# Kernel tuning notes

Hardware: AMD Instinct MI355X
Metric: run time of the kernel (lower is better)

Reference implementation:

```python
import jax, jax.numpy as jnp
import numpy as np
from jax import lax

B, T, C = 1, 2048, 2048
HS = 64
H = C // HS          # 32 heads
FFN = 7168
NS = 4               # packed sequences in the batch-1 stream
EPS_LN = 1e-5
EPS_GN = 1e-5 * 8 ** 2   # GroupNorm eps = 1e-5 * head_size_divisor**2


def setup_inputs() -> dict:
    key = jax.random.key(0)
    ks = iter(jax.random.split(key, 48))
    def rn(shape, s=1.0):
        return jax.random.normal(next(ks), shape, jnp.float32) * s
    sc = C ** -0.5
    return dict(
        x=rn((B, T, C)),
        start_pos=jnp.array([0, 512, 1024, 1536], dtype=jnp.int32),
        att_state=rn((NS, C)),
        wkv_state=rn((NS, H, HS, HS), 0.1),
        ffn_state=rn((NS, C)),
        ln1_g=jnp.ones((C,), jnp.float32), ln1_b=jnp.zeros((C,), jnp.float32),
        ln2_g=jnp.ones((C,), jnp.float32), ln2_b=jnp.zeros((C,), jnp.float32),
        tm_maa_x=rn((C,), 0.1), tm_maa_w=rn((C,), 0.1), tm_maa_k=rn((C,), 0.1),
        tm_maa_v=rn((C,), 0.1), tm_maa_r=rn((C,), 0.1), tm_maa_g=rn((C,), 0.1),
        tm_w1=rn((C, 160), 0.02), tm_w2=rn((5, 32, C), 0.02),
        td=rn((C,), 0.3) - 0.5, td_w1=rn((C, 64), 0.02), td_w2=rn((64, C), 0.02),
        u=rn((H, HS), 0.1),
        Wr=rn((C, C), sc), Wk=rn((C, C), sc), Wv=rn((C, C), sc),
        Wg=rn((C, C), sc), Wo=rn((C, C), sc),
        lnx_g=jnp.ones((C,), jnp.float32), lnx_b=jnp.zeros((C,), jnp.float32),
        cm_maa_k=rn((C,), 0.1), cm_maa_r=rn((C,), 0.1),
        Wck=rn((C, FFN), sc), Wcv=rn((FFN, C), FFN ** -0.5), Wcr=rn((C, C), sc),
    )


def _ln(x, g, b, eps):
    m = x.mean(-1, keepdims=True)
    v = ((x - m) ** 2).mean(-1, keepdims=True)
    return (x - m) * lax.rsqrt(v + eps) * g + b


def _shift(x, start_pos, state):
    # ZeroPad2d((0,0,1,-1)) token shift, then restore per-sequence carry state
    sh = jnp.concatenate([jnp.zeros_like(x[:, :1]), x[:, :-1]], axis=1)
    return sh.at[0, start_pos, :].set(state)


def reference(x, start_pos, att_state, wkv_state, ffn_state,
              ln1_g, ln1_b, ln2_g, ln2_b,
              tm_maa_x, tm_maa_w, tm_maa_k, tm_maa_v, tm_maa_r, tm_maa_g,
              tm_w1, tm_w2, td, td_w1, td_w2, u,
              Wr, Wk, Wv, Wg, Wo, lnx_g, lnx_b,
              cm_maa_k, cm_maa_r, Wck, Wcv, Wcr):
    is_start = jnp.zeros((T,), bool).at[start_pos].set(True)
    seq_id = jnp.clip(jnp.cumsum(is_start.astype(jnp.int32)) - 1, 0, NS - 1)

    # ---------------- Tmix (RWKV6 time mix) ----------------
    xa = _ln(x, ln1_g, ln1_b, EPS_LN)
    sh = _shift(xa, start_pos, att_state)
    xx = sh - xa
    xxx = jnp.tanh((xa + xx * tm_maa_x) @ tm_w1)                    # [B,T,160]
    mix = jnp.einsum('btse,sec->sbtc', xxx.reshape(B, T, 5, 32), tm_w2)
    mw, mk, mv, mr, mg = mix
    xw = xa + xx * (tm_maa_w + mw)
    xk = xa + xx * (tm_maa_k + mk)
    xv = xa + xx * (tm_maa_v + mv)
    xr = xa + xx * (tm_maa_r + mr)
    xg = xa + xx * (tm_maa_g + mg)
    r = (xr @ Wr).reshape(T, H, HS)
    k = (xk @ Wk).reshape(T, H, HS)
    v = (xv @ Wv).reshape(T, H, HS)
    g = jax.nn.silu(xg @ Wg)                                        # [B,T,C]
    w = td + jnp.tanh(xw @ td_w1) @ td_w2                           # [B,T,C]
    dec = jnp.exp(-jnp.exp(w)).reshape(T, H, HS)

    # continuous WKV recurrence: per-sequence state restore at starts
    def step(S, inp):
        rt, kt, vt, dt, st, sid = inp
        S = jnp.where(st, wkv_state[sid], S)                        # [H,HS,HS]
        y = jnp.einsum('hi,hij->hj', rt, S) \
            + (rt * u * kt).sum(-1, keepdims=True) * vt             # bonus term
        S = dt[:, :, None] * S + kt[:, :, None] * vt[:, None, :]
        return S, y

    _, y = lax.scan(step, jnp.zeros((H, HS, HS), jnp.float32),
                    (r, k, v, dec, is_start, seq_id))
    y = y.reshape(B, T, H, HS)
    # GroupNorm (n_head groups) fused per token/head
    mu = y.mean(-1, keepdims=True)
    var = ((y - mu) ** 2).mean(-1, keepdims=True)
    y = ((y - mu) * lax.rsqrt(var + EPS_GN)).reshape(B, T, C) * lnx_g + lnx_b
    x = x + (y * g) @ Wo

    # ---------------- CMix (channel mix) ----------------
    xf = _ln(x, ln2_g, ln2_b, EPS_LN)
    sh = _shift(xf, start_pos, ffn_state)
    xx = sh - xf
    xk = xf + xx * cm_maa_k
    xr = xf + xx * cm_maa_r
    kv = jnp.square(jax.nn.relu(xk @ Wck)) @ Wcv
    x = x + jax.nn.sigmoid(xr @ Wcr) * kv
    return x
```

## Files before the change

kernel.cpp:

```cpp
#include <hip/hip_runtime.h>
#include <stdint.h>


#define TT 2048
#define CC 2048
#define NH 32
#define HSZ 64
#define FFND 7168
#define CHUNK 32
#define NCHUNK 64

typedef __attribute__((ext_vector_type(8))) short short8;
typedef __attribute__((ext_vector_type(4))) float f32x4;

__device__ __forceinline__ float bf2f(short s){
  return __uint_as_float(((uint32_t)(uint16_t)s) << 16);
}
__device__ __forceinline__ short f2bf(float f){
  uint32_t u = __float_as_uint(f);
  u = u + 0x7fffu + ((u >> 16) & 1u);
  return (short)(u >> 16);
}

__global__ __launch_bounds__(256) void ln_kernel(
    const float* __restrict__ xin, const float* __restrict__ gam,
    const float* __restrict__ bet, float* __restrict__ out, float eps)
{
  int t = blockIdx.x, tid = threadIdx.x;
  const float* row = xin + (size_t)t*CC;
  float4 v0 = *(const float4*)(row + tid*8);
  float4 v1 = *(const float4*)(row + tid*8 + 4);
  float s  = v0.x+v0.y+v0.z+v0.w + v1.x+v1.y+v1.z+v1.w;
  float ss = v0.x*v0.x+v0.y*v0.y+v0.z*v0.z+v0.w*v0.w
           + v1.x*v1.x+v1.y*v1.y+v1.z*v1.z+v1.w*v1.w;
  #pragma unroll
  for(int off=1; off<64; off<<=1){ s += __shfl_xor(s,off); ss += __shfl_xor(ss,off); }
  __shared__ float sm[8];
  int w = tid>>6;
  if((tid&63)==0){ sm[w]=s; sm[4+w]=ss; }
  __syncthreads();
  s = sm[0]+sm[1]+sm[2]+sm[3]; ss = sm[4]+sm[5]+sm[6]+sm[7];
  float mean = s * (1.f/CC);
  float var  = ss * (1.f/CC) - mean*mean;
  float rstd = rsqrtf(var + eps);
  float* orow = out + (size_t)t*CC;
  int c = tid*8;
  float vv[8] = {v0.x,v0.y,v0.z,v0.w,v1.x,v1.y,v1.z,v1.w};
  #pragma unroll
  for(int j=0;j<8;j++) orow[c+j] = (vv[j]-mean)*rstd*gam[c+j] + bet[c+j];
}

__global__ __launch_bounds__(256) void ln2_fused_kernel(
    const float* __restrict__ p0, const float* __restrict__ p1,
    const float* __restrict__ xres, const float* __restrict__ gam,
    const float* __restrict__ bet, float* __restrict__ xsum,
    float* __restrict__ lnout, float eps)
{
  int t = blockIdx.x, tid = threadIdx.x;
  size_t base = (size_t)t*CC + tid*8;
  float vv[8];
  float s = 0.f, ss = 0.f;
  #pragma unroll
  for(int j=0;j<8;j++){
    float v = p0[base+j] + p1[base+j] + xres[base+j];
    vv[j] = v; s += v; ss += v*v;
    xsum[base+j] = v;
  }
  #pragma unroll
  for(int off=1; off<64; off<<=1){ s += __shfl_xor(s,off); ss += __shfl_xor(ss,off); }
  __shared__ float sm[8];
  int w = tid>>6;
  if((tid&63)==0){ sm[w]=s; sm[4+w]=ss; }
  __syncthreads();
  s = sm[0]+sm[1]+sm[2]+sm[3]; ss = sm[4]+sm[5]+sm[6]+sm[7];
  float mean = s * (1.f/CC);
  float var  = ss * (1.f/CC) - mean*mean;
  float rstd = rsqrtf(var + eps);
  int c = tid*8;
  #pragma unroll
  for(int j=0;j<8;j++) lnout[base+j] = (vv[j]-mean)*rstd*gam[c+j] + bet[c+j];
}

__global__ __launch_bounds__(256) void shift1_kernel(
    const float* __restrict__ xa, const float* __restrict__ st,
    const int* __restrict__ sp, float* __restrict__ xxb)
{
  int t = blockIdx.x, tid = threadIdx.x;
  int sp0=sp[0], sp1=sp[1], sp2=sp[2], sp3=sp[3];
  bool is_start = (sp0==t)|(sp1==t)|(sp2==t)|(sp3==t);
  int sid = (sp0<=t)+(sp1<=t)+(sp2<=t)+(sp3<=t) - 1;
  sid = sid<0?0:(sid>3?3:sid);
  int c = tid*8;
  const float* src = is_start ? (st + (size_t)sid*CC + c)
                   : (t>0 ? xa + (size_t)(t-1)*CC + c : nullptr);
  const float* cur = xa + (size_t)t*CC + c;
  float* o = xxb + (size_t)t*CC + c;
  #pragma unroll
  for(int jj=0;jj<8;jj++){
    float sh = src ? src[jj] : 0.f;
    o[jj] = sh - cur[jj];
  }
}

__global__ __launch_bounds__(256) void shift2_kernel(
    const float* __restrict__ xf, const float* __restrict__ st,
    const int* __restrict__ sp, const float* __restrict__ cmk,
    const float* __restrict__ cmr, short* __restrict__ xk2, short* __restrict__ xr2)
{
  int t = blockIdx.x, tid = threadIdx.x;
  int sp0=sp[0], sp1=sp[1], sp2=sp[2], sp3=sp[3];
  bool is_start = (sp0==t)|(sp1==t)|(sp2==t)|(sp3==t);
  int sid = (sp0<=t)+(sp1<=t)+(sp2<=t)+(sp3<=t) - 1;
  sid = sid<0?0:(sid>3?3:sid);
  int c = tid*8;
  const float* src = is_start ? (st + (size_t)sid*CC + c)
                   : (t>0 ? xf + (size_t)(t-1)*CC + c : nullptr);
  const float* cur = xf + (size_t)t*CC + c;
  size_t ix = (size_t)t*CC + c;
  #pragma unroll
  for(int jj=0;jj<8;jj++){
    float xfv = cur[jj];
    float sh = src ? src[jj] : 0.f;
    float d = sh - xfv;
    xk2[ix+jj] = f2bf(xfv + d*cmk[c+jj]);
    xr2[ix+jj] = f2bf(xfv + d*cmr[c+jj]);
  }
}

__global__ __launch_bounds__(256) void zprep_kernel(const float* __restrict__ xa,
   const float* __restrict__ xx, const float* __restrict__ maa, short* __restrict__ z)
{
  size_t i = ((size_t)blockIdx.x*256 + threadIdx.x)*8;
  int c = (int)(i & (CC-1));
  #pragma unroll
  for(int j=0;j<8;j++) z[i+j] = f2bf(xa[i+j] + xx[i+j]*maa[c+j]);
}

__global__ __launch_bounds__(256) void mix5_kernel(
    const float* __restrict__ xxxb, const float* __restrict__ w2,
    const float* __restrict__ xa, const float* __restrict__ xxv,
    const float* __restrict__ mw, const float* __restrict__ mk,
    const float* __restrict__ mv, const float* __restrict__ mr,
    const float* __restrict__ mg,
    short* __restrict__ ow, short* __restrict__ ok, short* __restrict__ ov,
    short* __restrict__ orr, short* __restrict__ og)
{
  int g = blockIdx.x*256 + threadIdx.x;
  int c = g & (CC-1);
  int t0 = (g >> 11) * 8;
  float acc[5][8];
  #pragma unroll
  for(int s=0;s<5;s++)
    #pragma unroll
    for(int tt=0;tt<8;tt++) acc[s][tt]=0.f;
  #pragma unroll
  for(int s=0;s<5;s++){
    for(int e=0;e<32;e++){
      float wv = w2[(size_t)(s*32+e)*CC + c];
      #pragma unroll
      for(int tt=0;tt<8;tt++)
        acc[s][tt] += xxxb[(size_t)(t0+tt)*160 + s*32 + e] * wv;
    }
  }
  float vmw=mw[c], vmk=mk[c], vmv=mv[c], vmr=mr[c], vmg=mg[c];
  #pragma unroll
  for(int tt=0;tt<8;tt++){
    size_t ix = (size_t)(t0+tt)*CC + c;
    float av = xa[ix], xv = xxv[ix];
    ow[ix]  = f2bf(av + xv*(vmw + acc[0][tt]));
    ok[ix]  = f2bf(av + xv*(vmk + acc[1][tt]));
    ov[ix]  = f2bf(av + xv*(vmv + acc[2][tt]));
    orr[ix] = f2bf(av + xv*(vmr + acc[3][tt]));
    og[ix]  = f2bf(av + xv*(vmg + acc[4][tt]));
  }
}

__global__ __launch_bounds__(256) void dec_kernel(
    const float* __restrict__ h1b, const float* __restrict__ tw2,
    const float* __restrict__ td, float* __restrict__ out)
{
  int g = blockIdx.x*256 + threadIdx.x;
  int c = g & (CC-1);
  int t0 = (g >> 11)*8;
  float acc[8] = {0,0,0,0,0,0,0,0};
  for(int e=0;e<64;e++){
    float wv = tw2[(size_t)e*CC + c];
    #pragma unroll
    for(int tt=0;tt<8;tt++) acc[tt] += h1b[(size_t)(t0+tt)*64 + e]*wv;
  }
  float tdc = td[c];
  #pragma unroll
  for(int tt=0;tt<8;tt++)
    out[(size_t)(t0+tt)*CC + c] = expf(-expf(tdc + acc[tt]));
}

template<int N, int NK>
__global__ __launch_bounds__(256) void tanh_reduce_kernel(
    const float* __restrict__ part, float* __restrict__ out)
{
  int idx = blockIdx.x*256 + threadIdx.x;
  int col = idx & (N-1);
  int row = idx >> (N==256 ? 8 : 7);
  float s = 0.f;
  #pragma unroll
  for(int z=0;z<8;z++) s += part[(size_t)z*TT*N + idx];
  if(col < NK) out[(size_t)row*NK + col] = tanhf(s);
}

__global__ __launch_bounds__(256) void transpose_f2bf_kernel(
    const float* __restrict__ W, short* __restrict__ Wt, int K, int N)
{
  __shared__ float tile[64][65];
  int n0 = blockIdx.x*64, k0 = blockIdx.y*64;
  int tid = threadIdx.x;
  #pragma unroll
  for(int q=0;q<16;q++){
    int ix = q*256 + tid;
    int r = ix >> 6, cc2 = ix & 63;
    tile[r][cc2] = (n0 + cc2 < N) ? W[(size_t)(k0+r)*N + n0 + cc2] : 0.f;
  }
  __syncthreads();
  #pragma unroll
  for(int q=0;q<16;q++){
    int ix = q*256 + tid;
    int r = ix >> 6, cc2 = ix & 63;
    Wt[(size_t)(n0+r)*K + k0 + cc2] = f2bf(tile[cc2][r]);
  }
}

struct WPtr4 { const float* w[4]; };
__global__ __launch_bounds__(256) void transpose4_f2bf_kernel(
    WPtr4 ws4, short* __restrict__ Wt)
{
  __shared__ float tile[64][65];
  int z = blockIdx.z;
  const float* W = ws4.w[z];
  short* dst = Wt + (size_t)z*CC*CC;
  int n0 = blockIdx.x*64, k0 = blockIdx.y*64;
  int tid = threadIdx.x;
  #pragma unroll
  for(int q=0;q<16;q++){
    int ix = q*256 + tid;
    int r = ix >> 6, cc2 = ix & 63;
    tile[r][cc2] = W[(size_t)(k0+r)*CC + n0 + cc2];
  }
  __syncthreads();
  #pragma unroll
  for(int q=0;q<16;q++){
    int ix = q*256 + tid;
    int r = ix >> 6, cc2 = ix & 63;
    dst[(size_t)(n0+r)*CC + k0 + cc2] = f2bf(tile[cc2][r]);
  }
}

__device__ __forceinline__ void load_lds16(const void* g, void* l){
  __builtin_amdgcn_global_load_lds(
      (const __attribute__((address_space(1))) uint32_t*)g,
      (__attribute__((address_space(3))) uint32_t*)l, 16, 0, 0);
}

template<int EPI>
__global__ __launch_bounds__(256) void gemm_bt_kernel(
    const short* __restrict__ A, const short* __restrict__ Bt,
    void* __restrict__ Cout, int M, int N, int Kstride, int Klen,
    long zA, long zB, long zC)
{
  __shared__ __align__(16) short As[128*64];
  __shared__ __align__(16) short Bs[128*64];
  int z = blockIdx.z;
  const short* A0 = A + (size_t)z*zA;
  const short* B0 = Bt + (size_t)z*zB;
  int tid = threadIdx.x;
  int w = tid >> 6, lane = tid & 63;
  int l16 = lane & 15, lhi = lane >> 4;
  int wr = w >> 1, wc = w & 1;
  int gx = gridDim.x;
  int nwg = gx*gridDim.y;
  int lin = blockIdx.y*gx + blockIdx.x;
  int wg = (lin & 7)*(nwg >> 3) + (lin >> 3);
  int bn = wg % gx, bm = wg / gx;
  const short* Ab = A0 + (size_t)bm*128*Kstride;
  const short* Bb = B0 + (size_t)bn*128*Kstride;
  int srow = w*8 + (lane>>3);
  int scol = lane & 7;
  f32x4 acc[4][4] = {};
  for(int kt=0; kt<Klen; kt+=64){
    __syncthreads();
    #pragma unroll
    for(int q=0;q<4;q++){
      int row = q*32 + srow;
      int c8 = scol ^ (row & 7);
      int ldsoff = (q*256 + w*64)*8;
      load_lds16(Ab + (size_t)row*Kstride + kt + c8*8, As + ldsoff);
      load_lds16(Bb + (size_t)row*Kstride + kt + c8*8, Bs + ldsoff);
    }
    __syncthreads();
    #pragma unroll
    for(int kk=0;kk<2;kk++){
      short8 af[4], bf[4];
      #pragma unroll
      for(int m=0;m<4;m++){
        int row = wr*64 + m*16 + l16;
        int slot = (kk*4 + lhi) ^ (row & 7);
        af[m] = *(const short8*)(As + row*64 + slot*8);
      }
      #pragma unroll
      for(int n=0;n<4;n++){
        int row = wc*64 + n*16 + l16;
        int slot = (kk*4 + lhi) ^ (row & 7);
        bf[n] = *(const short8*)(Bs + row*64 + slot*8);
      }
      #pragma unroll
      for(int m=0;m<4;m++){
        #pragma unroll
        for(int n=0;n<4;n++)
          acc[m][n] = __builtin_amdgcn_mfma_f32_16x16x32_bf16(af[m], bf[n], acc[m][n], 0, 0, 0);
      }
    }
  }
  int m0 = bm*128 + wr*64;
  int n0 = bn*128 + wc*64;
  #pragma unroll
  for(int m=0;m<4;m++){
    #pragma unroll
    for(int n=0;n<4;n++){
      #pragma unroll
      for(int jj=0;jj<4;jj++){
        int row = m0 + m*16 + lhi*4 + jj;
        int col = n0 + n*16 + l16;
        size_t ix = (size_t)row*N + col;
        float val = acc[m][n][jj];
        if constexpr (EPI==0){ ((short*)Cout)[(size_t)z*zC + ix] = f2bf(val); }
        else if constexpr (EPI==3){ float rv = fmaxf(val, 0.f); ((short*)Cout)[ix] = f2bf(rv*rv); }
        else if constexpr (EPI==5){ ((float*)Cout)[(size_t)z*zC + ix] = val; }
        else {
          short* o = (short*)Cout + (size_t)z*zC;
          o[ix] = (z==3) ? f2bf(val/(1.f+expf(-val))) : f2bf(val);
        }
      }
    }
  }
}

__global__ __launch_bounds__(256) void wkv_chunk_kernel(
    const short* __restrict__ rb, const short* __restrict__ kb,
    const short* __restrict__ vb, const float* __restrict__ db,
    const float* __restrict__ wkv_state, const float* __restrict__ u,
    const int* __restrict__ sp,
    float* __restrict__ yb, short* __restrict__ rtb,
    float* __restrict__ Bc, float* __restrict__ Pc)
{
  int blk = blockIdx.x;
  int ch = blk >> 5;
  int h  = blk & 31;
  int tid = threadIdx.x;
  int a = tid & 3, j = tid >> 2;
  int w = tid >> 6, lane = tid & 63;
  __shared__ float sr[2][64], sk[2][64], suk[2][64], sv[2][64], sd[2][64];
  __shared__ float sp_[64];
  float u_reg = (w==1) ? u[h*64 + lane] : 0.f;
  if(tid < 64) sp_[tid] = 1.f;
  float S[16];
  #pragma unroll
  for(int ii=0;ii<16;ii++) S[ii]=0.f;
  int sp0=sp[0], sp1=sp[1], sp2=sp[2], sp3=sp[3];
  int tbase = ch*CHUNK;
  {
    size_t gb = (size_t)tbase*CC + h*64;
    if(w==0)      sr[0][lane] = bf2f(rb[gb+lane]);
    else if(w==1){ float kv_=bf2f(kb[gb+lane]); sk[0][lane]=kv_; suk[0][lane]=u_reg*kv_; }
    else if(w==2) sv[0][lane] = bf2f(vb[gb+lane]);
    else          sd[0][lane] = db[gb+lane];
  }
  __syncthreads();
  for(int tl=0; tl<CHUNK; ++tl){
    int t = tbase + tl;
    int buf = tl & 1;
    if(tl+1 < CHUNK){
      size_t nb = (size_t)(t+1)*CC + h*64;
      int b2_ = buf^1;
      if(w==0)      sr[b2_][lane] = bf2f(rb[nb+lane]);
      else if(w==1){ float kv_=bf2f(kb[nb+lane]); sk[b2_][lane]=kv_; suk[b2_][lane]=u_reg*kv_; }
      else if(w==2) sv[b2_][lane] = bf2f(vb[nb+lane]);
      else          sd[b2_][lane] = db[nb+lane];
    }
    size_t base = (size_t)t*CC + h*64;
    bool is_start = (sp0==t)|(sp1==t)|(sp2==t)|(sp3==t);
    if(is_start){
      int sid = (sp0<=t)+(sp1<=t)+(sp2<=t)+(sp3<=t) - 1;
      sid = sid<0?0:(sid>3?3:sid);
      const float* wsrc = wkv_state + (((size_t)sid*NH + h)*HSZ + a*16)*HSZ + j;
      #pragma unroll
      for(int ii=0;ii<16;ii++) S[ii] = wsrc[(size_t)ii*HSZ];
      if(tid < 64) sp_[tid] = 0.f;
    }
    float vj = sv[buf][j];
    float yp = 0.f, bp = 0.f;
    #pragma unroll
    for(int ii=0;ii<16;ii++){
      int i = a*16 + ii;
      float ri = sr[buf][i];
      yp += ri * S[ii];
      bp += ri * suk[buf][i];
    }
    yp += __shfl_xor(yp, 1); yp += __shfl_xor(yp, 2);
    bp += __shfl_xor(bp, 1); bp += __shfl_xor(bp, 2);
    if(a == 0) yb[base + j] = yp + bp*vj;
    if(tid < 64){
      rtb[base + tid] = f2bf(sr[buf][tid] * sp_[tid]);
      sp_[tid] *= sd[buf][tid];
    }
    #pragma unroll
    for(int ii=0;ii<16;ii++){
      int i = a*16 + ii;
      S[ii] = sd[buf][i]*S[ii] + sk[buf][i]*vj;
    }
    __syncthreads();
  }
  size_t cb = ((size_t)ch*NH + h)*HSZ*HSZ;
  #pragma unroll
  for(int ii=0;ii<16;ii++) Bc[cb + (size_t)(a*16+ii)*HSZ + j] = S[ii];
  if(tid < 64) Pc[((size_t)ch*NH + h)*HSZ + tid] = sp_[tid];
}

__global__ __launch_bounds__(256) void wkv_combine_kernel(
    float* __restrict__ BS, const float* __restrict__ Pc)
{
  int idx = blockIdx.x*256 + threadIdx.x;
  int hi = idx >> 6;
  float s = 0.f;
  for(int cc=0; cc<NCHUNK; ++cc){
    size_t ix = (size_t)cc*(NH*HSZ*HSZ) + idx;
    float b = BS[ix];
    BS[ix] = s;
    s = Pc[cc*(NH*HSZ) + hi]*s + b;
  }
}

__global__ __launch_bounds__(256) void wkv_corr_kernel(
    const short* __restrict__ rtb, const float* __restrict__ Sin, float* __restrict__ yb)
{
  int blk = blockIdx.x;
  int ch = blk >> 5, h = blk & 31;
  __shared__ float Ssm[64][64];
  __shared__ float Rsm[32][65];
  int tid = threadIdx.x;
  const float* Sp = Sin + (size_t)(ch*NH + h)*HSZ*HSZ;
  #pragma unroll
  for(int q=0;q<16;q++) ((float*)Ssm)[q*256+tid] = Sp[q*256+tid];
  #pragma unroll
  for(int q=0;q<8;q++){
    int ix = q*256 + tid;
    int tl = ix>>6, i = ix&63;
    Rsm[tl][i] = bf2f(rtb[(size_t)(ch*CHUNK+tl)*CC + h*64 + i]);
  }
  __syncthreads();
  int tl = tid >> 3;
  int jq = tid & 7;
  float acc[8];
  #pragma unroll
  for(int jj=0;jj<8;jj++) acc[jj]=0.f;
  for(int i=0;i<64;i++){
    float rv = Rsm[tl][i];
    #pragma unroll
    for(int jj=0;jj<8;jj++) acc[jj] += rv * Ssm[i][jq*8+jj];
  }
  #pragma unroll
  for(int jj=0;jj<8;jj++)
    yb[(size_t)(ch*CHUNK+tl)*CC + h*64 + jq*8+jj] += acc[jj];
}

__global__ __launch_bounds__(256) void gn_mul_kernel(
    const float* __restrict__ yb, const short* __restrict__ gb,
    const float* __restrict__ gam, const float* __restrict__ bet,
    short* __restrict__ yg)
{
  int t = blockIdx.x, tid = threadIdx.x;
  int w = tid >> 6, lane = tid & 63;
  for(int q=0;q<8;q++){
    int h = q*4 + w;
    int cc = h*64 + lane;
    float val = yb[(size_t)t*CC + cc];
    float s = val, ss = val*val;
    #pragma unroll
    for(int off=1;off<64;off<<=1){ s += __shfl_xor(s,off); ss += __shfl_xor(ss,off); }
    float mu = s*(1.f/64.f);
    float var = ss*(1.f/64.f) - mu*mu;
    float rstd = rsqrtf(var + 6.4e-4f);
    float o = (val-mu)*rstd*gam[cc] + bet[cc];
    yg[(size_t)t*CC + cc] = f2bf(o * bf2f(gb[(size_t)t*CC + cc]));
  }
}

__global__ __launch_bounds__(256) void final_kernel(
    const float* __restrict__ s0, const float* __restrict__ s1,
    const float* __restrict__ kv0, const float* __restrict__ kv1,
    float* __restrict__ out)
{
  size_t i = ((size_t)blockIdx.x*256 + threadIdx.x)*8;
  #pragma unroll
  for(int j=0;j<8;j++){
    float sv = s0[i+j] + s1[i+j];
    float sig = 1.f/(1.f + expf(-sv));
    out[i+j] = out[i+j] + sig*(kv0[i+j] + kv1[i+j]);
  }
}

extern "C" void kernel_launch(void* const* d_in, const int* in_sizes, int n_in,
                              void* d_out, int out_size, void* d_ws, size_t ws_size,
                              hipStream_t stream)
{
  (void)in_sizes; (void)n_in; (void)out_size;
  const float* x         = (const float*)d_in[0];
  const int*   sp        = (const int*)d_in[1];
  const float* att_state = (const float*)d_in[2];
  const float* wkv_state = (const float*)d_in[3];
  const float* ffn_state = (const float*)d_in[4];
  const float* ln1_g=(const float*)d_in[5],  *ln1_b=(const float*)d_in[6];
  const float* ln2_g=(const float*)d_in[7],  *ln2_b=(const float*)d_in[8];
  const float* maa_x=(const float*)d_in[9],  *maa_w=(const float*)d_in[10], *maa_k=(const float*)d_in[11];
  const float* maa_v=(const float*)d_in[12], *maa_r=(const float*)d_in[13], *maa_g=(const float*)d_in[14];
  const float* tm_w1=(const float*)d_in[15], *tm_w2=(const float*)d_in[16];
  const float* td=(const float*)d_in[17],    *td_w1=(const float*)d_in[18], *td_w2=(const float*)d_in[19];
  const float* u = (const float*)d_in[20];
  const float* Wr=(const float*)d_in[21], *Wk=(const float*)d_in[22], *Wv=(const float*)d_in[23];
  const float* Wg=(const float*)d_in[24], *Wo=(const float*)d_in[25];
  const float* lnx_g=(const float*)d_in[26], *lnx_b=(const float*)d_in[27];
  const float* cm_k=(const float*)d_in[28],  *cm_r=(const float*)d_in[29];
  const float* Wck=(const float*)d_in[30], *Wcv=(const float*)d_in[31], *Wcr=(const float*)d_in[32];

  char* ws = (char*)d_ws;
  const size_t SLOT  = (size_t)TT*CC*4;
  const size_t BSLOT = (size_t)TT*CC*2;
  const size_t WT_SZ = (size_t)4*CC*CC*2;
  const size_t NEED  = 6*SLOT + 10*BSLOT + WT_SZ + (4u<<20);
  if(ws_size < NEED) return;

  float* xa   = (float*)(ws + 0*SLOT);
  float* xxb  = (float*)(ws + 1*SLOT);
  float* zw   = (float*)(ws + 2*SLOT);
  float* decb = (float*)(ws + 3*SLOT);
  float* yb   = (float*)(ws + 4*SLOT);
  float* S5   = (float*)(ws + 5*SLOT);
  float* BS   = xa;
  float* xxxPart = zw;
  float* h1Part  = yb;
  short* bA   = (short*)(ws + 6*SLOT);
  short* bO   = (short*)(ws + 6*SLOT + 4*BSLOT);
  short* b1 = bO + 0*(TT*CC);
  short* b2 = bO + 1*(TT*CC);
  short* b3 = bO + 2*(TT*CC);
  short* b4 = bO + 3*(TT*CC);
  short* b5 = bO + 4*(TT*CC);
  short* b6 = bO + 5*(TT*CC);
  short* WT = (short*)(ws + 6*SLOT + 10*BSLOT);
  char*  aux = (char*)WT + WT_SZ;
  float* xxxb = (float*)(aux);
  float* h1b  = (float*)(aux + (2u<<20));
  float* Pc   = (float*)(aux + (5u<<19));
  float* xmid = (float*)d_out;

  dim3 B256(256);
  const int NTC8 = TT*CC/8/256;

  ln_kernel<<<TT, B256, 0, stream>>>(x, ln1_g, ln1_b, xa, 1e-5f);
  shift1_kernel<<<TT, B256, 0, stream>>>(xa, att_state, sp, xxb);
  zprep_kernel<<<NTC8, B256, 0, stream>>>(xa, xxb, maa_x, bA);
  transpose_f2bf_kernel<<<dim3(4, CC/64), B256, 0, stream>>>(tm_w1, WT, CC, 160);
  gemm_bt_kernel<5><<<dim3(2, TT/128, 8), B256, 0, stream>>>(bA, WT, xxxPart, TT, 256, CC, 256,
      256, 256, (long)TT*256);
  tanh_reduce_kernel<256,160><<<TT, B256, 0, stream>>>(xxxPart, xxxb);
  mix5_kernel<<<NTC8, B256, 0, stream>>>(xxxb, tm_w2, xa, xxb,
      maa_w, maa_k, maa_v, maa_r, maa_g,
      b5, bA + 1*(TT*CC), bA + 2*(TT*CC), bA, bA + 3*(TT*CC));
  transpose_f2bf_kernel<<<dim3(2, CC/64), B256, 0, stream>>>(td_w1, WT, CC, 64);
  gemm_bt_kernel<5><<<dim3(1, TT/128, 8), B256, 0, stream>>>(b5, WT, h1Part, TT, 128, CC, 256,
      256, 256, (long)TT*128);
  tanh_reduce_kernel<128,64><<<TT/2, B256, 0, stream>>>(h1Part, h1b);
  dec_kernel<<<NTC8, B256, 0, stream>>>(h1b, td_w2, td, decb);

  WPtr4 w4; w4.w[0]=Wr; w4.w[1]=Wk; w4.w[2]=Wv; w4.w[3]=Wg;
  transpose4_f2bf_kernel<<<dim3(CC/64, CC/64, 4), B256, 0, stream>>>(w4, WT);
  gemm_bt_kernel<6><<<dim3(CC/128, TT/128, 4), B256, 0, stream>>>(bA, WT, b1, TT, CC, CC, CC,
      (long)TT*CC, (long)CC*CC, (long)TT*CC);

  wkv_chunk_kernel<<<NCHUNK*NH, B256, 0, stream>>>(b1, b2, b3, decb, wkv_state, u, sp,
                                                   yb, b5, BS, Pc);
  wkv_combine_kernel<<<NH*HSZ*HSZ/256, B256, 0, stream>>>(BS, Pc);
  wkv_corr_kernel<<<NCHUNK*NH, B256, 0, stream>>>(b5, BS, yb);
  gn_mul_kernel<<<TT, B256, 0, stream>>>(yb, b4, lnx_g, lnx_b, b6);

  transpose_f2bf_kernel<<<dim3(CC/64, CC/64), B256, 0, stream>>>(Wo, WT, CC, CC);
  gemm_bt_kernel<5><<<dim3(CC/128, TT/128, 2), B256, 0, stream>>>(b6, WT, yb, TT, CC, CC, 1024,
      1024, 1024, (long)TT*CC);
  ln2_fused_kernel<<<TT, B256, 0, stream>>>(yb, S5, x, ln2_g, ln2_b, xmid, zw, 1e-5f);

  shift2_kernel<<<TT, B256, 0, stream>>>(zw, ffn_state, sp, cm_k, cm_r, bA, bA + 1*(TT*CC));
  transpose_f2bf_kernel<<<dim3(FFND/64, CC/64), B256, 0, stream>>>(Wck, WT, CC, FFND);
  gemm_bt_kernel<3><<<dim3(FFND/128, TT/128, 1), B256, 0, stream>>>(bA, WT, b1, TT, FFND, CC, CC, 0,0,0);
  transpose_f2bf_kernel<<<dim3(CC/64, FFND/64), B256, 0, stream>>>(Wcv, WT, FFND, CC);
  gemm_bt_kernel<5><<<dim3(CC/128, TT/128, 2), B256, 0, stream>>>(b1, WT, yb, TT, CC, FFND, 3584,
      3584, 3584, (long)TT*CC);
  transpose_f2bf_kernel<<<dim3(CC/64, CC/64), B256, 0, stream>>>(Wcr, WT, CC, CC);
  gemm_bt_kernel<5><<<dim3(CC/128, TT/128, 2), B256, 0, stream>>>(bA + 1*(TT*CC), WT, xa, TT, CC, CC, 1024,
      1024, 1024, (long)TT*CC);
  final_kernel<<<NTC8, B256, 0, stream>>>(xa, xxb, yb, S5, xmid);
}
```

Measured before the change: 845.1 us.

## Add 256x256-tile 512-thread GEMM for projection and FFN GEMMs, widen split-K

Adds a new bf16 MFMA GEMM kernel that uses 256x256 output tiles, 512 threads, double-buffered swizzled LDS and an XCD-aware workgroup remap. It replaces the 128-tile GEMM for the fused R/K/V/G projection, the FFN key GEMM and the FFN value GEMM. The FFN value GEMM now splits K four ways instead of two, and the final kernel sums four partial buffers. The larger tiles are meant to raise data reuse per LDS load and cut global traffic. In exchange the launch uses fewer workgroups, each limited to one block per CU, and extra partial buffers must be written and read. It also reuses workspace buffers (zw, decb) as the extra partials.

```diff
diff --git a/kernel.cpp b/kernel.cpp
--- a/kernel.cpp
+++ b/kernel.cpp
@@ -342,6 +342,119 @@
   }
 }
 
+template<int EPI>
+__global__ __launch_bounds__(512, 1) void gemm256_kernel(
+    const short* __restrict__ A, const short* __restrict__ Bt,
+    void* __restrict__ Cout, int M, int N, int Kstride, int Klen,
+    long zA, long zB, long zC)
+{
+  __shared__ __align__(16) short As[2][256*64];
+  __shared__ __align__(16) short Bs[2][256*64];
+  int z = blockIdx.z;
+  const short* A0 = A + (size_t)z*zA;
+  const short* B0 = Bt + (size_t)z*zB;
+  int tid = threadIdx.x;
+  int w = tid >> 6, lane = tid & 63;
+  int l16 = lane & 15, lhi = lane >> 4;
+  int wr = w >> 2, wc = w & 3;
+  int gx = gridDim.x;
+  int nwg = gx*gridDim.y;
+  int lin = blockIdx.y*gx + blockIdx.x;
+  int wg = (lin & 7)*(nwg >> 3) + (lin >> 3);
+  int bn = wg % gx, bm = wg / gx;
+  const short* Ab = A0 + (size_t)bm*256*Kstride;
+  const short* Bb = B0 + (size_t)bn*256*Kstride;
+  int srow_w = w*8 + (lane>>3);
+  int scol = lane & 7;
+  f32x4 acc[8][4] = {};
+
+  auto STAGE = [&](int kt, int b){
+    #pragma unroll
+    for(int q=0;q<4;q++){
+      int row = q*64 + srow_w;
+      int c8 = scol ^ (row & 7);
+      int ldsoff = (q*64 + w*8)*64;
+      load_lds16(Ab + (size_t)row*Kstride + kt + c8*8, &As[b][ldsoff]);
+      load_lds16(Bb + (size_t)row*Kstride + kt + c8*8, &Bs[b][ldsoff]);
+    }
+  };
+
+  int NT = Klen >> 6;
+  int cur = 0;
+  STAGE(0, 0);
+  for(int t=0; t<NT; ++t){
+    __builtin_amdgcn_sched_barrier(0);
+    if(t+1 < NT){
+      STAGE((t+1)<<6, cur^1);
+      asm volatile("s_waitcnt vmcnt(8)" ::: "memory");
+    } else {
+      asm volatile("s_waitcnt vmcnt(0)" ::: "memory");
+    }
+    __builtin_amdgcn_s_barrier();
+    __builtin_amdgcn_sched_barrier(0);
+    const short* Ac = &As[cur][0];
+    const short* Bc = &Bs[cur][0];
+    short8 bfr[4][2];
+    #pragma unroll
+    for(int n=0;n<4;n++){
+      #pragma unroll
+      for(int kk=0;kk<2;kk++){
+        int row = wc*64 + n*16 + l16;
+        int slot = (kk*4 + lhi) ^ (row & 7);
+        bfr[n][kk] = *(const short8*)(Bc + row*64 + slot*8);
+      }
+    }
+    #pragma unroll
+    for(int p=0;p<4;p++){
+      short8 afr[2][2];
+      #pragma unroll
+      for(int mm=0;mm<2;mm++){
+        #pragma unroll
+        for(int kk=0;kk<2;kk++){
+          int row = wr*128 + (p*2+mm)*16 + l16;
+          int slot = (kk*4 + lhi) ^ (row & 7);
+          afr[mm][kk] = *(const short8*)(Ac + row*64 + slot*8);
+        }
+      }
+      __builtin_amdgcn_s_setprio(1);
+      #pragma unroll
+      for(int mm=0;mm<2;mm++){
+        #pragma unroll
+        for(int n=0;n<4;n++){
+          #pragma unroll
+          for(int kk=0;kk<2;kk++)
+            acc[p*2+mm][n] = __builtin_amdgcn_mfma_f32_16x16x32_bf16(
+                afr[mm][kk], bfr[n][kk], acc[p*2+mm][n], 0, 0, 0);
+        }
+      }
+      __builtin_amdgcn_s_setprio(0);
+      __builtin_amdgcn_s_barrier();
+    }
+    cur ^= 1;
+  }
+  int m0 = bm*256 + wr*128;
+  int n0 = bn*256 + wc*64;
+  #pragma unroll
+  for(int m=0;m<8;m++){
+    #pragma unroll
+    for(int n=0;n<4;n++){
+      #pragma unroll
+      for(int jj=0;jj<4;jj++){
+        int row = m0 + m*16 + lhi*4 + jj;
+        int col = n0 + n*16 + l16;
+        size_t ix = (size_t)row*N + col;
+        float val = acc[m][n][jj];
+        if constexpr (EPI==3){ float rv = fmaxf(val, 0.f); ((short*)Cout)[ix] = f2bf(rv*rv); }
+        else if constexpr (EPI==5){ ((float*)Cout)[(size_t)z*zC + ix] = val; }
+        else {
+          short* o = (short*)Cout + (size_t)z*zC;
+          o[ix] = (z==3) ? f2bf(val/(1.f+expf(-val))) : f2bf(val);
+        }
+      }
+    }
+  }
+}
+
 __global__ __launch_bounds__(256) void wkv_chunk_kernel(
     const short* __restrict__ rb, const short* __restrict__ kb,
     const short* __restrict__ vb, const float* __restrict__ db,
@@ -495,6 +608,7 @@
 __global__ __launch_bounds__(256) void final_kernel(
     const float* __restrict__ s0, const float* __restrict__ s1,
     const float* __restrict__ kv0, const float* __restrict__ kv1,
+    const float* __restrict__ kv2, const float* __restrict__ kv3,
     float* __restrict__ out)
 {
   size_t i = ((size_t)blockIdx.x*256 + threadIdx.x)*8;
@@ -502,7 +616,7 @@
   for(int j=0;j<8;j++){
     float sv = s0[i+j] + s1[i+j];
     float sig = 1.f/(1.f + expf(-sv));
-    out[i+j] = out[i+j] + sig*(kv0[i+j] + kv1[i+j]);
+    out[i+j] = out[i+j] + sig*(kv0[i+j] + kv1[i+j] + kv2[i+j] + kv3[i+j]);
   }
 }
 
@@ -560,7 +674,7 @@
   float* Pc   = (float*)(aux + (5u<<19));
   float* xmid = (float*)d_out;
 
-  dim3 B256(256);
+  dim3 B256(256), B512(512);
   const int NTC8 = TT*CC/8/256;
 
   ln_kernel<<<TT, B256, 0, stream>>>(x, ln1_g, ln1_b, xa, 1e-5f);
@@ -581,7 +695,7 @@
 
   WPtr4 w4; w4.w[0]=Wr; w4.w[1]=Wk; w4.w[2]=Wv; w4.w[3]=Wg;
   transpose4_f2bf_kernel<<<dim3(CC/64, CC/64, 4), B256, 0, stream>>>(w4, WT);
-  gemm_bt_kernel<6><<<dim3(CC/128, TT/128, 4), B256, 0, stream>>>(bA, WT, b1, TT, CC, CC, CC,
+  gemm256_kernel<6><<<dim3(CC/256, TT/256, 4), B512, 0, stream>>>(bA, WT, b1, TT, CC, CC, CC,
       (long)TT*CC, (long)CC*CC, (long)TT*CC);
 
   wkv_chunk_kernel<<<NCHUNK*NH, B256, 0, stream>>>(b1, b2, b3, decb, wkv_state, u, sp,
@@ -597,12 +711,13 @@
 
   shift2_kernel<<<TT, B256, 0, stream>>>(zw, ffn_state, sp, cm_k, cm_r, bA, bA + 1*(TT*CC));
   transpose_f2bf_kernel<<<dim3(FFND/64, CC/64), B256, 0, stream>>>(Wck, WT, CC, FFND);
-  gemm_bt_kernel<3><<<dim3(FFND/128, TT/128, 1), B256, 0, stream>>>(bA, WT, b1, TT, FFND, CC, CC, 0,0,0);
+  gemm256_kernel<3><<<dim3(FFND/256, TT/256, 1), B512, 0, stream>>>(bA, WT, b1, TT, FFND, CC, CC,
+      0, 0, 0);
   transpose_f2bf_kernel<<<dim3(CC/64, FFND/64), B256, 0, stream>>>(Wcv, WT, FFND, CC);
-  gemm_bt_kernel<5><<<dim3(CC/128, TT/128, 2), B256, 0, stream>>>(b1, WT, yb, TT, CC, FFND, 3584,
-      3584, 3584, (long)TT*CC);
+  gemm256_kernel<5><<<dim3(CC/256, TT/256, 4), B512, 0, stream>>>(b1, WT, zw, TT, CC, FFND, 1792,
+      1792, 1792, (long)TT*CC);
   transpose_f2bf_kernel<<<dim3(CC/64, CC/64), B256, 0, stream>>>(Wcr, WT, CC, CC);
   gemm_bt_kernel<5><<<dim3(CC/128, TT/128, 2), B256, 0, stream>>>(bA + 1*(TT*CC), WT, xa, TT, CC, CC, 1024,
       1024, 1024, (long)TT*CC);
-  final_kernel<<<NTC8, B256, 0, stream>>>(xa, xxb, yb, S5, xmid);
-}
+  final_kernel<<<NTC8, B256, 0, stream>>>(xa, xxb, zw, decb, yb, S5, xmid);
+}
```

Result: faster. 792.4 us (-6.2%).
